# Kernel optimization log

Measured on AMD Instinct MI355X. Metric: run time of the kernel, lower is better.

## Reference

```python
import jax, jax.numpy as jnp
import numpy as np

N_FEAT = 1024
N_HEAD = 8
CONTEXT_SIZES = [21, 41]
HPS = N_HEAD // len(CONTEXT_SIZES)  # heads per scale = 4


def setup_inputs() -> dict:
    key = jax.random.key(0)
    ks = jax.random.split(key, 9)
    B, T, D = 4, 1024, N_FEAT
    s = 1.0 / np.sqrt(D)
    return {
        "query": jax.random.normal(ks[0], (B, T, D), dtype=jnp.float32),
        "key": jax.random.normal(ks[1], (B, T, D), dtype=jnp.float32),
        "value": jax.random.normal(ks[2], (B, T, D), dtype=jnp.float32),
        # weights stored [in, out] (torch Linear applies x @ W.T)
        "W_qv": jax.random.normal(ks[3], (D, 2 * D), dtype=jnp.float32) * s,
        "W2_0": jax.random.normal(ks[4], (D, HPS * CONTEXT_SIZES[0]), dtype=jnp.float32) * s,
        "W2_1": jax.random.normal(ks[5], (D, HPS * CONTEXT_SIZES[1]), dtype=jnp.float32) * s,
        "scale_weights": jnp.ones((len(CONTEXT_SIZES),), dtype=jnp.float32) / len(CONTEXT_SIZES),
        "W_out": jax.random.normal(ks[6], (D, D), dtype=jnp.float32) * s,
    }


def _sliding_window(v, c):
    # v: [B, T, D] -> [B, T, c, D], symmetric zero pad of (c-1)//2 each side
    B, T, D = v.shape
    half = (c - 1) // 2
    v_pad = jnp.pad(v, ((0, 0), (half, half), (0, 0)))
    idx = jnp.arange(T)[:, None] + jnp.arange(c)[None, :]  # [T, c]
    return v_pad[:, idx]  # [B, T, c, D]


def reference(query, key, value, W_qv, W2_0, W2_1, scale_weights, W_out):
    B, T, D = query.shape
    qv = query @ W_qv                      # [B, T, 2D]
    q, v = jnp.split(qv, 2, axis=-1)       # each [B, T, D]
    sw = jax.nn.softmax(scale_weights)     # [n_scales]
    head_dim = D // HPS
    x = jnp.zeros_like(query)
    for i, (c, W2) in enumerate(zip(CONTEXT_SIZES, [W2_0, W2_1])):
        # synthesized attention logits: [B, T, HPS, c]
        logits = (jax.nn.relu(q) @ W2).reshape(B, T, HPS, c)
        attn = jax.nn.softmax(logits, axis=-1)
        vw = _sliding_window(v, c).reshape(B, T, c, HPS, head_dim)
        out = jnp.einsum('bthc,btchd->bthd', attn, vw).reshape(B, T, D)
        x = x + sw[i] * out
    return x @ W_out
```

## Files before the change

### kernel.cpp

```cpp
#include <hip/hip_runtime.h>
#include <hip/hip_bf16.h>
#include <math.h>

#define BB 4
#define TT 1024
#define DD 1024
#define HPS 4
#define C0 21
#define C1 41
#define N0 (HPS * C0)
#define N1 (HPS * C1)
#define NL 256
#define BT (BB * TT)
#define TB 64
#define HALO 20
#define HB (TB + 2 * HALO)
#define KSPLIT 2

typedef unsigned int uint;
typedef __bf16 bf16x8 __attribute__((ext_vector_type(8)));
typedef float f32x4 __attribute__((ext_vector_type(4)));

__device__ __forceinline__ ushort f2bf(float f) {
    union { float f; uint u; } v; v.f = f;
    uint u = v.u;
    uint r = (u + 0x7FFFu + ((u >> 16) & 1u)) >> 16;
    return (ushort)r;
}
__device__ __forceinline__ float bf2f(ushort s) {
    union { uint u; float f; } v; v.u = ((uint)s) << 16;
    return v.f;
}

#define RQ  4096
#define R1  (RQ + 2048)
#define R2  (R1 + 1024)
#define R3  (R2 + 96)
#define R4  (R3 + 192)

__device__ __forceinline__ void transpose_tile(
    const float* __restrict__ in, ushort* __restrict__ out,
    int K, int Nin, int n_base, int Npad, int nx, int ky, int tid)
{
    __shared__ float tile[32][33];
    const int tx = tid & 31;
    const int ty = tid >> 5;
    const int n0 = nx * 32;
    const int k0 = ky * 32;
    #pragma unroll
    for (int i = 0; i < 4; i++) {
        int k = k0 + ty + i * 8;
        int n = n0 + tx;
        float v = (k < K && n < Nin) ? in[(size_t)k * Nin + n] : 0.0f;
        tile[ty + i * 8][tx] = v;
    }
    __syncthreads();
    #pragma unroll
    for (int i = 0; i < 4; i++) {
        int n = n0 + ty + i * 8;
        int k = k0 + tx;
        if (n < Npad && k < K)
            out[(size_t)(n_base + n) * K + k] = f2bf(tile[tx][ty + i * 8]);
    }
}

__global__ __launch_bounds__(256) void convert_all(
    const float* __restrict__ query, ushort* __restrict__ query_bf,
    const float* __restrict__ W_qv,  ushort* __restrict__ WqvT,
    const float* __restrict__ W_out, ushort* __restrict__ WoutT,
    const float* __restrict__ W2_0, const float* __restrict__ W2_1,
    ushort* __restrict__ W2T)
{
    const int blk = blockIdx.x;
    const int tid = threadIdx.x;
    if (blk < RQ) {
        int i = blk * 1024 + tid * 4;
        float4 v = *(const float4*)(query + i);
        ushort4 o;
        o.x = f2bf(v.x); o.y = f2bf(v.y); o.z = f2bf(v.z); o.w = f2bf(v.w);
        *(ushort4*)(query_bf + i) = o;
    } else if (blk < R1) {
        int idx = blk - RQ;
        transpose_tile(W_qv, WqvT, DD, 2 * DD, 0, 2 * DD, idx & 63, idx >> 6, tid);
    } else if (blk < R2) {
        int idx = blk - R1;
        transpose_tile(W_out, WoutT, DD, DD, 0, DD, idx & 31, idx >> 5, tid);
    } else if (blk < R3) {
        int idx = blk - R2;
        transpose_tile(W2_0, W2T, DD, N0, 0, N0, idx % 3, idx / 3, tid);
    } else {
        int idx = blk - R3;
        transpose_tile(W2_1, W2T, DD, N1, N0, NL - N0, idx % 6, idx / 6, tid);
    }
}

__global__ __launch_bounds__(256) void gemm_mfma(
    const ushort* __restrict__ A, const ushort* __restrict__ Bt,
    int K, int klen,
    float* __restrict__ Cf, ushort* __restrict__ Cb, ushort* __restrict__ Cv,
    int mode, int ldc)
{
    __shared__ ushort As[128 * 128];
    __shared__ ushort Bs[128 * 128];

    const int tid = threadIdx.x;
    const int wv  = tid >> 6;
    const int ln  = tid & 63;
    const int row0 = blockIdx.y * 128;
    const int col0 = blockIdx.x * 128;
    const int kbase = blockIdx.z * klen;
    const int wr = (wv >> 1) * 64;
    const int wc = (wv & 1) * 64;
    const int l15 = ln & 15;
    const int lq  = ln >> 4;

    f32x4 acc[4][4];
    #pragma unroll
    for (int i = 0; i < 4; i++)
        #pragma unroll
        for (int j = 0; j < 4; j++)
            acc[i][j] = (f32x4){0.f, 0.f, 0.f, 0.f};

    const int r_lo = wv * 4 + (ln >> 4);
    const int cc   = (ln & 15) ^ (r_lo & 7);
    const ushort* gA = A  + (size_t)(row0 + r_lo) * K + kbase + cc * 8;
    const ushort* gB = Bt + (size_t)(col0 + r_lo) * K + kbase + cc * 8;

    const int fx = l15 & 7;

    for (int k0 = 0; k0 < klen; k0 += 128) {
        __syncthreads();
        #pragma unroll
        for (int i = 0; i < 8; i++) {
            __builtin_amdgcn_global_load_lds(
                (const __attribute__((address_space(1))) void*)(gA + (size_t)i * 16 * K + k0),
                (__attribute__((address_space(3))) void*)(As + i * 2048 + wv * 512),
                16, 0, 0);
        }
        #pragma unroll
        for (int i = 0; i < 8; i++) {
            __builtin_amdgcn_global_load_lds(
                (const __attribute__((address_space(1))) void*)(gB + (size_t)i * 16 * K + k0),
                (__attribute__((address_space(3))) void*)(Bs + i * 2048 + wv * 512),
                16, 0, 0);
        }
        __syncthreads();

        #pragma unroll
        for (int s = 0; s < 4; s++) {
            const int ca = ((s * 4 + lq) ^ fx) * 8;
            bf16x8 af[4], bfr[4];
            #pragma unroll
            for (int mi = 0; mi < 4; mi++)
                af[mi] = *(const bf16x8*)&As[(wr + mi * 16 + l15) * 128 + ca];
            #pragma unroll
            for (int ni = 0; ni < 4; ni++)
                bfr[ni] = *(const bf16x8*)&Bs[(wc + ni * 16 + l15) * 128 + ca];
            #pragma unroll
            for (int mi = 0; mi < 4; mi++)
                #pragma unroll
                for (int ni = 0; ni < 4; ni++)
                    acc[mi][ni] = __builtin_amdgcn_mfma_f32_16x16x32_bf16(
                        af[mi], bfr[ni], acc[mi][ni], 0, 0, 0);
        }
    }

    #pragma unroll
    for (int mi = 0; mi < 4; mi++) {
        #pragma unroll
        for (int ni = 0; ni < 4; ni++) {
            #pragma unroll
            for (int r = 0; r < 4; r++) {
                int row = row0 + wr + mi * 16 + lq * 4 + r;
                int col = col0 + wc + ni * 16 + l15;
                float v = acc[mi][ni][r];
                if (mode == 0) {
                    Cf[(size_t)row * ldc + col] = v;
                } else if (mode == 2) {
                    if (col < DD) Cb[(size_t)row * DD + col] = f2bf(fmaxf(v, 0.0f));
                    else          Cv[(size_t)row * DD + (col - DD)] = f2bf(v);
                } else {
                    Cf[((size_t)blockIdx.z * BT + row) * ldc + col] = v;
                }
            }
        }
    }
}

__global__ __launch_bounds__(256) void attn_window_kernel(
    const ushort* __restrict__ v,
    const float* __restrict__ Lp,
    const float* __restrict__ scale_w,
    ushort* __restrict__ x)
{
    const int blk = blockIdx.x;
    const int h  = blk & 3;
    const int tt = (blk >> 2) & 15;
    const int b  = blk >> 6;
    const int t0 = tt * TB;
    const int tid = threadIdx.x;
    const size_t PS = (size_t)BT * NL;

    __shared__ ushort vs[HB][256];
    __shared__ float  cw[TB][42];

    const ushort* vb = v + (size_t)b * TT * DD + h * 256;
    #pragma unroll
    for (int i = 0; i < 13; i++) {
        int c = i * 256 + tid;
        int r = c >> 5;
        int cir = c & 31;
        int t = t0 - HALO + r;
        uint4 val = make_uint4(0, 0, 0, 0);
        if (t >= 0 && t < TT)
            val = *(const uint4*)(vb + (size_t)t * DD + cir * 8);
        *(uint4*)(&vs[r][cir * 8]) = val;
    }

    if (tid < TB) {
        const int bt = b * TT + t0 + tid;
        const float* Lb = Lp + (size_t)bt * NL;

        float s0 = scale_w[0], s1 = scale_w[1];
        float mm = fmaxf(s0, s1);
        float e0 = __expf(s0 - mm), e1 = __expf(s1 - mm);
        float inv01 = 1.0f / (e0 + e1);
        float sw0 = e0 * inv01, sw1 = e1 * inv01;

        float w0[C0], w1[C1];
        {
            const int off = h * C0;
            float m = -1e30f;
            #pragma unroll
            for (int j = 0; j < C0; j++) {
                w0[j] = Lb[off + j] + Lb[PS + off + j];
                m = fmaxf(m, w0[j]);
            }
            float s = 0.0f;
            #pragma unroll
            for (int j = 0; j < C0; j++) { w0[j] = __expf(w0[j] - m); s += w0[j]; }
            float inv = sw0 / s;
            #pragma unroll
            for (int j = 0; j < C0; j++) w0[j] *= inv;
        }
        {
            const int off = N0 + h * C1;
            float m = -1e30f;
            #pragma unroll
            for (int j = 0; j < C1; j++) {
                w1[j] = Lb[off + j] + Lb[PS + off + j];
                m = fmaxf(m, w1[j]);
            }
            float s = 0.0f;
            #pragma unroll
            for (int j = 0; j < C1; j++) { w1[j] = __expf(w1[j] - m); s += w1[j]; }
            float inv = sw1 / s;
            #pragma unroll
            for (int j = 0; j < C1; j++) w1[j] *= inv;
        }
        #pragma unroll
        for (int o = 0; o < C1; o++) {
            float w = w1[o];
            if (o >= 10 && o <= 30) w += w0[o - 10];
            cw[tid][o] = w;
        }
    }
    __syncthreads();

    const int tq = tid >> 6;
    const int dg = tid & 63;
    const int d  = dg * 4;

    for (int tloc = 0; tloc < 16; tloc++) {
        const int tp = tq * 16 + tloc;
        f32x4 acc = {0.f, 0.f, 0.f, 0.f};
        #pragma unroll
        for (int o = 0; o < C1; o++) {
            float w = cw[tp][o];
            ushort4 vv = *(const ushort4*)(&vs[tp + o][d]);
            acc[0] = fmaf(w, bf2f(vv.x), acc[0]);
            acc[1] = fmaf(w, bf2f(vv.y), acc[1]);
            acc[2] = fmaf(w, bf2f(vv.z), acc[2]);
            acc[3] = fmaf(w, bf2f(vv.w), acc[3]);
        }
        const int bt = b * TT + t0 + tp;
        ushort4 o4;
        o4.x = f2bf(acc[0]); o4.y = f2bf(acc[1]);
        o4.z = f2bf(acc[2]); o4.w = f2bf(acc[3]);
        *(ushort4*)(x + (size_t)bt * DD + h * 256 + d) = o4;
    }
}

extern "C" void kernel_launch(void* const* d_in, const int* in_sizes, int n_in,
                              void* d_out, int out_size, void* d_ws, size_t ws_size,
                              hipStream_t stream)
{
    const float* query   = (const float*)d_in[0];
    const float* W_qv    = (const float*)d_in[3];
    const float* W2_0    = (const float*)d_in[4];
    const float* W2_1    = (const float*)d_in[5];
    const float* scale_w = (const float*)d_in[6];
    const float* W_out   = (const float*)d_in[7];
    float* out = (float*)d_out;

    char* ws = (char*)d_ws;
    ushort* W2T      = (ushort*)ws;                 ws += (size_t)NL * DD * 2;
    ushort* WoutT    = (ushort*)ws;                 ws += (size_t)DD * DD * 2;
    ushort* query_bf = (ushort*)ws;
    float*  logitsP  = (float*)ws;                  ws += (size_t)BT * DD * 2;
    ushort* WqvT     = (ushort*)ws;                 ws += (size_t)2 * DD * DD * 2;
    ushort* reluq    = (ushort*)ws;                 ws += (size_t)BT * DD * 2;
    ushort* vbuf     = (ushort*)ws;                 ws += (size_t)BT * DD * 2;
    ushort* xbuf     = (ushort*)ws;                 ws += (size_t)BT * DD * 2;

    convert_all<<<R4, 256, 0, stream>>>(query, query_bf, W_qv, WqvT,
                                        W_out, WoutT, W2_0, W2_1, W2T);

    {   dim3 grid(2 * DD / 128, BT / 128, 1);
        gemm_mfma<<<grid, 256, 0, stream>>>(query_bf, WqvT, DD, DD,
                                            nullptr, reluq, vbuf, 2, 0); }
    {   dim3 grid(NL / 128, BT / 128, KSPLIT);
        gemm_mfma<<<grid, 256, 0, stream>>>(reluq, W2T, DD, DD / KSPLIT,
                                            logitsP, nullptr, nullptr, 3, NL); }
    attn_window_kernel<<<256, 256, 0, stream>>>(vbuf, logitsP, scale_w, xbuf);

    {   dim3 grid(DD / 128, BT / 128, 1);
        gemm_mfma<<<grid, 256, 0, stream>>>(xbuf, WoutT, DD, DD,
                                            out, nullptr, nullptr, 0, DD); }
}
```

Measured before the change: 199.9 us.

## Double-buffer LDS tiles in bf16 MFMA GEMM with BK=64 prefetch

```diff
diff --git a/kernel.cpp b/kernel.cpp
--- a/kernel.cpp
+++ b/kernel.cpp
@@ -16,6 +16,7 @@
 #define HALO 20
 #define HB (TB + 2 * HALO)
 #define KSPLIT 2
+#define BK 64
 
 typedef unsigned int uint;
 typedef __bf16 bf16x8 __attribute__((ext_vector_type(8)));
@@ -100,8 +101,8 @@
     float* __restrict__ Cf, ushort* __restrict__ Cb, ushort* __restrict__ Cv,
     int mode, int ldc)
 {
-    __shared__ ushort As[128 * 128];
-    __shared__ ushort Bs[128 * 128];
+    __shared__ ushort As[2][128 * BK];
+    __shared__ ushort Bs[2][128 * BK];
 
     const int tid = threadIdx.x;
     const int wv  = tid >> 6;
@@ -121,41 +122,43 @@
         for (int j = 0; j < 4; j++)
             acc[i][j] = (f32x4){0.f, 0.f, 0.f, 0.f};
 
-    const int r_lo = wv * 4 + (ln >> 4);
-    const int cc   = (ln & 15) ^ (r_lo & 7);
-    const ushort* gA = A  + (size_t)(row0 + r_lo) * K + kbase + cc * 8;
-    const ushort* gB = Bt + (size_t)(col0 + r_lo) * K + kbase + cc * 8;
+    const int r_in = wv * 32 + (ln >> 3);
+    const int cg   = (ln & 7) ^ (ln >> 3);
+    const ushort* gA = A  + (size_t)(row0 + r_in) * K + kbase + cg * 8;
+    const ushort* gB = Bt + (size_t)(col0 + r_in) * K + kbase + cg * 8;
 
     const int fx = l15 & 7;
 
-    for (int k0 = 0; k0 < klen; k0 += 128) {
-        __syncthreads();
-        #pragma unroll
-        for (int i = 0; i < 8; i++) {
+    const int nt = klen / BK;
+
+    auto STAGE = [&](int buf, int kk) {
+        #pragma unroll
+        for (int i = 0; i < 4; i++) {
             __builtin_amdgcn_global_load_lds(
-                (const __attribute__((address_space(1))) void*)(gA + (size_t)i * 16 * K + k0),
-                (__attribute__((address_space(3))) void*)(As + i * 2048 + wv * 512),
+                (const __attribute__((address_space(1))) void*)(gA + (size_t)i * 8 * K + kk),
+                (__attribute__((address_space(3))) void*)(&As[buf][(wv * 32 + i * 8) * BK]),
                 16, 0, 0);
         }
         #pragma unroll
-        for (int i = 0; i < 8; i++) {
+        for (int i = 0; i < 4; i++) {
             __builtin_amdgcn_global_load_lds(
-                (const __attribute__((address_space(1))) void*)(gB + (size_t)i * 16 * K + k0),
-                (__attribute__((address_space(3))) void*)(Bs + i * 2048 + wv * 512),
+                (const __attribute__((address_space(1))) void*)(gB + (size_t)i * 8 * K + kk),
+                (__attribute__((address_space(3))) void*)(&Bs[buf][(wv * 32 + i * 8) * BK]),
                 16, 0, 0);
         }
-        __syncthreads();
-
-        #pragma unroll
-        for (int s = 0; s < 4; s++) {
+    };
+
+    auto COMPUTE = [&](int buf) {
+        #pragma unroll
+        for (int s = 0; s < 2; s++) {
             const int ca = ((s * 4 + lq) ^ fx) * 8;
             bf16x8 af[4], bfr[4];
             #pragma unroll
             for (int mi = 0; mi < 4; mi++)
-                af[mi] = *(const bf16x8*)&As[(wr + mi * 16 + l15) * 128 + ca];
+                af[mi] = *(const bf16x8*)&As[buf][(wr + mi * 16 + l15) * BK + ca];
             #pragma unroll
             for (int ni = 0; ni < 4; ni++)
-                bfr[ni] = *(const bf16x8*)&Bs[(wc + ni * 16 + l15) * 128 + ca];
+                bfr[ni] = *(const bf16x8*)&Bs[buf][(wc + ni * 16 + l15) * BK + ca];
             #pragma unroll
             for (int mi = 0; mi < 4; mi++)
                 #pragma unroll
@@ -163,6 +166,17 @@
                     acc[mi][ni] = __builtin_amdgcn_mfma_f32_16x16x32_bf16(
                         af[mi], bfr[ni], acc[mi][ni], 0, 0, 0);
         }
+    };
+
+    int cur = 0;
+    STAGE(0, 0);
+    __syncthreads();
+    for (int t = 0; t < nt; ++t) {
+        const bool more = (t + 1 < nt);
+        if (more) STAGE(cur ^ 1, (t + 1) * BK);
+        COMPUTE(cur);
+        if (more) __syncthreads();
+        cur ^= 1;
     }
 
     #pragma unroll
```

After: 201.2 us. No clear change (+0.7%).
